# Kernel optimization log

Hardware: AMD Instinct MI355X
Metric: run time of the kernel (lower is better)

Reference implementation:

```python
import jax, jax.numpy as jnp
import numpy as np

N = 100000      # num nodes
E = 1600000     # num edges
IN, H, OUT = 128, 64, 64
EPS = 1e-5      # BatchNorm eps


def setup_inputs() -> dict:
    key = jax.random.key(0)
    ks = jax.random.split(key, 12)
    x = jax.random.normal(ks[0], (N, IN), dtype=jnp.float32)
    edge_index = jax.random.randint(ks[1], (2, E), 0, N, dtype=jnp.int64)
    def lin(k, fan_in, fan_out):
        s = 1.0 / np.sqrt(fan_in)
        kw, kb = jax.random.split(k)
        W = jax.random.uniform(kw, (fan_in, fan_out), jnp.float32, -s, s)
        b = jax.random.uniform(kb, (fan_out,), jnp.float32, -s, s)
        return W, b
    W1, b1 = lin(ks[2], IN, H)
    W2, b2 = lin(ks[3], H, H)
    W3, b3 = lin(ks[4], H, OUT)
    g1 = jnp.ones((H,), jnp.float32); beta1 = jnp.zeros((H,), jnp.float32)
    g2 = jnp.ones((H,), jnp.float32); beta2 = jnp.zeros((H,), jnp.float32)
    rm1 = 0.1 * jax.random.normal(ks[5], (H,), jnp.float32)
    rv1 = 1.0 + 0.1 * jax.random.uniform(ks[6], (H,), jnp.float32)
    rm2 = 0.1 * jax.random.normal(ks[7], (H,), jnp.float32)
    rv2 = 1.0 + 0.1 * jax.random.uniform(ks[8], (H,), jnp.float32)
    return dict(x=x, edge_index=edge_index, W1=W1, b1=b1, W2=W2, b2=b2,
                W3=W3, b3=b3, g1=g1, beta1=beta1, rm1=rm1, rv1=rv1,
                g2=g2, beta2=beta2, rm2=rm2, rv2=rv2)


def _gcn_conv(x, W, b, src, dst, edge_coef, self_coef):
    # x' = D^{-1/2}(A+I)D^{-1/2} (x W) + b   (GCNConv with self-loops)
    h = x @ W                                           # [N, F_out]
    msgs = h[src] * edge_coef[:, None]                  # gather + scale [E, F_out]
    agg = jax.ops.segment_sum(msgs, dst, num_segments=N)  # scatter-add
    return agg + h * self_coef[:, None] + b


def _bn_eval(x, g, beta, rm, rv):
    return (x - rm) * jax.lax.rsqrt(rv + EPS) * g + beta


def reference(x, edge_index, W1, b1, W2, b2, W3, b3,
              g1, beta1, rm1, rv1, g2, beta2, rm2, rv2):
    src, dst = edge_index[0], edge_index[1]
    # symmetric normalization coefficients (deg includes self-loop)
    deg = jax.ops.segment_sum(jnp.ones((E,), x.dtype), dst, num_segments=N) + 1.0
    dinv = jax.lax.rsqrt(deg)
    edge_coef = dinv[src] * dinv[dst]   # [E]
    self_coef = dinv * dinv             # [N]

    h = _gcn_conv(x, W1, b1, src, dst, edge_coef, self_coef)
    h = jax.nn.relu(_bn_eval(h, g1, beta1, rm1, rv1))   # dropout = identity (eval)
    h = _gcn_conv(h, W2, b2, src, dst, edge_coef, self_coef)
    h = jax.nn.relu(_bn_eval(h, g2, beta2, rm2, rv2))
    return _gcn_conv(h, W3, b3, src, dst, edge_coef, self_coef)
```

## Files before the change

### kernel.cpp

```cpp
#include <hip/hip_runtime.h>
#include <hip/hip_fp16.h>

#define NN 100000
#define EE 1600000
#define K1 128
#define HH 64

#define NB 196
#define BW 512
#define CAP 12288
#define CHUNK 4096


__global__ void k_zeroB(int* __restrict__ bcursor) {
    bcursor[threadIdx.x] = 0;
}

__global__ __launch_bounds__(256) void k_binA(const int* __restrict__ ei,
                                              int* __restrict__ bcursor,
                                              uint2* __restrict__ binned) {
    __shared__ int lh[256], lbase[256], lcur[256];
    int t = threadIdx.x;
    int e0 = blockIdx.x * CHUNK;
    int e1 = min(e0 + CHUNK, EE);
    lh[t] = 0;
    __syncthreads();
    for (int e = e0 + t; e < e1; e += 256) {
        int d = ei[EE + e];
        atomicAdd(&lh[d >> 9], 1);
    }
    __syncthreads();
    lbase[t] = (lh[t] > 0) ? atomicAdd(&bcursor[t], lh[t]) : 0;
    lcur[t] = 0;
    __syncthreads();
    for (int e = e0 + t; e < e1; e += 256) {
        int s = ei[e];
        int d = ei[EE + e];
        int b = d >> 9;
        int pos = lbase[b] + atomicAdd(&lcur[b], 1);
        binned[(size_t)b * CAP + pos] = make_uint2((unsigned)s, (unsigned)d);
    }
}

__global__ __launch_bounds__(256) void k_sortB(const uint2* __restrict__ binned,
                                               const int* __restrict__ bcursor,
                                               int* __restrict__ offsets,
                                               float* __restrict__ dinv,
                                               int* __restrict__ csr_src) {
    __shared__ int lhist[BW], excl[BW], lcur[BW];
    __shared__ int sbase_sm;
    int t = threadIdx.x;
    int b = blockIdx.x;
    int lo = b << 9;
    int cnt = bcursor[b];

    lcur[t] = (t < b) ? bcursor[t] : 0;
    __syncthreads();
    for (int off = 128; off > 0; off >>= 1) {
        if (t < off) lcur[t] += lcur[t + off];
        __syncthreads();
    }
    if (t == 0) sbase_sm = lcur[0];
    for (int j = t; j < BW; j += 256) lhist[j] = 0;
    __syncthreads();
    int sbase = sbase_sm;
    const uint2* bp = binned + (size_t)b * CAP;
    for (int i = t; i < cnt; i += 256)
        atomicAdd(&lhist[bp[i].y - lo], 1);
    __syncthreads();
    if (t < 64) {
        int v[8], s = 0;
#pragma unroll
        for (int i = 0; i < 8; i++) { v[i] = lhist[t * 8 + i]; s += v[i]; }
        int run = s;
        for (int off = 1; off < 64; off <<= 1) {
            int u = __shfl_up(run, off);
            if (t >= off) run += u;
        }
        int base = run - s;
#pragma unroll
        for (int i = 0; i < 8; i++) { excl[t * 8 + i] = base; base += v[i]; }
    }
    __syncthreads();
    for (int j = t; j < BW; j += 256) {
        int d = lo + j;
        if (d < NN) {
            offsets[d] = sbase + excl[j];
            dinv[d] = rsqrtf((float)lhist[j] + 1.0f);
        }
    }
    if (b == NB - 1 && t == 0) offsets[NN] = sbase + cnt;
    for (int j = t; j < BW; j += 256) lcur[j] = 0;
    __syncthreads();
    for (int i = t; i < cnt; i += 256) {
        uint2 u = bp[i];
        int d = (int)u.y - lo;
        int slot = excl[d] + atomicAdd(&lcur[d], 1);
        csr_src[sbase + slot] = (int)u.x;
    }
}


template <int K, int TM, bool INH>
__global__ __launch_bounds__(256) void k_gemm(const void* __restrict__ xin,
                                              const float* __restrict__ W,
                                              __half* __restrict__ h) {
    __shared__ float Wl[K * 64];
    __shared__ float xs[TM * K];
    int t = threadIdx.x;
    int base = blockIdx.x * TM;
    for (int i = t; i < K * 16; i += 256)
        reinterpret_cast<float4*>(Wl)[i] = reinterpret_cast<const float4*>(W)[i];
    {
        const int NF4 = TM * K / 4;
        const int RF4 = K / 4;
        for (int i = t; i < NF4; i += 256) {
            int r = i / RF4, c = i - r * RF4;
            int gr = base + r; if (gr >= NN) gr = NN - 1;
            float4 v;
            if (INH) {
                uint2 u = reinterpret_cast<const uint2*>(xin)[(size_t)gr * RF4 + c];
                const __half2* hh = reinterpret_cast<const __half2*>(&u);
                float2 f01 = __half22float2(hh[0]);
                float2 f23 = __half22float2(hh[1]);
                v = make_float4(f01.x, f01.y, f23.x, f23.y);
            } else {
                v = reinterpret_cast<const float4*>(xin)[(size_t)gr * RF4 + c];
            }
            reinterpret_cast<float4*>(xs)[i] = v;
        }
    }
    __syncthreads();

    int lane = t & 63;
    int wid = t >> 6;
    const int RW = TM / 4;
    int r0 = wid * RW;
    float acc[RW];
#pragma unroll
    for (int r = 0; r < RW; r++) acc[r] = 0.f;

    for (int k = 0; k < K; k += 4) {
        float w0 = Wl[(k + 0) * 64 + lane];
        float w1 = Wl[(k + 1) * 64 + lane];
        float w2 = Wl[(k + 2) * 64 + lane];
        float w3 = Wl[(k + 3) * 64 + lane];
#pragma unroll
        for (int r = 0; r < RW; r++) {
            const float4 xv = *reinterpret_cast<const float4*>(&xs[(r0 + r) * K + k]);
            acc[r] = fmaf(xv.x, w0, acc[r]);
            acc[r] = fmaf(xv.y, w1, acc[r]);
            acc[r] = fmaf(xv.z, w2, acc[r]);
            acc[r] = fmaf(xv.w, w3, acc[r]);
        }
    }
    __half* hp = h + ((size_t)base + r0) * 64 + lane;
#pragma unroll
    for (int r = 0; r < RW; r++)
        if (base + r0 + r < NN) hp[r * 64] = __float2half(acc[r]);
}


template <bool BN, bool OUTH>
__global__ __launch_bounds__(256) void k_agg(const __half* __restrict__ h,
                                             const int* __restrict__ csr_src,
                                             const int* __restrict__ offsets,
                                             const float* __restrict__ dinv,
                                             const float* __restrict__ bias,
                                             const float* __restrict__ g,
                                             const float* __restrict__ beta,
                                             const float* __restrict__ rm,
                                             const float* __restrict__ rv,
                                             void* __restrict__ outp) {
    int node = (blockIdx.x * 256 + threadIdx.x) >> 6;
    int lane = threadIdx.x & 63;
    int q = lane >> 4;
    int p = lane & 15;
    int start = offsets[node];
    int len = offsets[node + 1] - start;
    const int* ep = csr_src + start;
    const uint2* hp = reinterpret_cast<const uint2*>(h);

    float a0 = 0.f, a1 = 0.f, a2 = 0.f, a3 = 0.f;
    int i = 0;
    for (; i + 16 <= len; i += 16) {
        uint2 dv[4]; float cf[4];
#pragma unroll
        for (int s = 0; s < 4; s++) {
            int srcn = __builtin_nontemporal_load(ep + i + 4 * q + s);
            cf[s] = dinv[srcn];
            dv[s] = hp[(size_t)srcn * 16 + p];
        }
#pragma unroll
        for (int s = 0; s < 4; s++) {
            const __half2* hh = reinterpret_cast<const __half2*>(&dv[s]);
            float2 f01 = __half22float2(hh[0]);
            float2 f23 = __half22float2(hh[1]);
            a0 = fmaf(f01.x, cf[s], a0);
            a1 = fmaf(f01.y, cf[s], a1);
            a2 = fmaf(f23.x, cf[s], a2);
            a3 = fmaf(f23.y, cf[s], a3);
        }
    }
    if (i < len) {
        uint2 dv[4]; float cf[4];
#pragma unroll
        for (int s = 0; s < 4; s++) {
            int slot = i + 4 * q + s;
            int cl = slot < len ? slot : len - 1;
            int srcn = __builtin_nontemporal_load(ep + cl);
            cf[s] = (slot < len) ? dinv[srcn] : 0.f;
            dv[s] = hp[(size_t)srcn * 16 + p];
        }
#pragma unroll
        for (int s = 0; s < 4; s++) {
            const __half2* hh = reinterpret_cast<const __half2*>(&dv[s]);
            float2 f01 = __half22float2(hh[0]);
            float2 f23 = __half22float2(hh[1]);
            a0 = fmaf(f01.x, cf[s], a0);
            a1 = fmaf(f01.y, cf[s], a1);
            a2 = fmaf(f23.x, cf[s], a2);
            a3 = fmaf(f23.y, cf[s], a3);
        }
    }
    a0 += __shfl_xor(a0, 16); a0 += __shfl_xor(a0, 32);
    a1 += __shfl_xor(a1, 16); a1 += __shfl_xor(a1, 32);
    a2 += __shfl_xor(a2, 16); a2 += __shfl_xor(a2, 32);
    a3 += __shfl_xor(a3, 16); a3 += __shfl_xor(a3, 32);

    if (q == 0) {
        uint2 sv = hp[(size_t)node * 16 + p];
        const __half2* sh = reinterpret_cast<const __half2*>(&sv);
        float2 s01 = __half22float2(sh[0]);
        float2 s23 = __half22float2(sh[1]);
        float di = dinv[node];
        float d2 = di * di;
        float4 bi = reinterpret_cast<const float4*>(bias)[p];
        float r0 = fmaf(s01.x, d2, a0 * di) + bi.x;
        float r1 = fmaf(s01.y, d2, a1 * di) + bi.y;
        float r2 = fmaf(s23.x, d2, a2 * di) + bi.z;
        float r3 = fmaf(s23.y, d2, a3 * di) + bi.w;
        if (BN) {
            float4 gv = reinterpret_cast<const float4*>(g)[p];
            float4 bv = reinterpret_cast<const float4*>(beta)[p];
            float4 mv = reinterpret_cast<const float4*>(rm)[p];
            float4 vv = reinterpret_cast<const float4*>(rv)[p];
            r0 = fmaxf(fmaf(r0 - mv.x, gv.x * rsqrtf(vv.x + 1e-5f), bv.x), 0.f);
            r1 = fmaxf(fmaf(r1 - mv.y, gv.y * rsqrtf(vv.y + 1e-5f), bv.y), 0.f);
            r2 = fmaxf(fmaf(r2 - mv.z, gv.z * rsqrtf(vv.z + 1e-5f), bv.z), 0.f);
            r3 = fmaxf(fmaf(r3 - mv.w, gv.w * rsqrtf(vv.w + 1e-5f), bv.w), 0.f);
        }
        if (OUTH) {
            __half2 o01, o23;
            o01.x = __float2half_rn(r0); o01.y = __float2half_rn(r1);
            o23.x = __float2half_rn(r2); o23.y = __float2half_rn(r3);
            uint2 o;
            o.x = *reinterpret_cast<unsigned*>(&o01);
            o.y = *reinterpret_cast<unsigned*>(&o23);
            reinterpret_cast<uint2*>(outp)[(size_t)node * 16 + p] = o;
        } else {
            float4 o = make_float4(r0, r1, r2, r3);
            reinterpret_cast<float4*>(outp)[(size_t)node * 16 + p] = o;
        }
    }
}


extern "C" void kernel_launch(void* const* d_in, const int* in_sizes, int n_in,
                              void* d_out, int out_size, void* d_ws, size_t ws_size,
                              hipStream_t stream) {
    const float* x = (const float*)d_in[0];
    const int* ei = (const int*)d_in[1];
    const float* W1 = (const float*)d_in[2];
    const float* b1 = (const float*)d_in[3];
    const float* W2 = (const float*)d_in[4];
    const float* b2 = (const float*)d_in[5];
    const float* W3 = (const float*)d_in[6];
    const float* b3 = (const float*)d_in[7];
    const float* g1 = (const float*)d_in[8];
    const float* be1 = (const float*)d_in[9];
    const float* rm1 = (const float*)d_in[10];
    const float* rv1 = (const float*)d_in[11];
    const float* g2 = (const float*)d_in[12];
    const float* be2 = (const float*)d_in[13];
    const float* rm2 = (const float*)d_in[14];
    const float* rv2 = (const float*)d_in[15];
    float* out = (float*)d_out;

    char* ws = (char*)d_ws;
    size_t off = 0;
    auto alloc = [&](size_t bytes) -> void* {
        void* p = ws + off;
        off = (off + bytes + 255) & ~(size_t)255;
        return p;
    };
    int* bcursor = (int*)alloc(256 * 4);
    int* offsets = (int*)alloc((size_t)(NN + 1) * 4);
    float* dinv = (float*)alloc((size_t)NN * 4);
    uint2* binned = (uint2*)alloc((size_t)NB * CAP * 8);
    int* csr_src = (int*)alloc((size_t)EE * 4);
    __half* h16 = (__half*)alloc((size_t)NN * 64 * 2);
    __half* y16 = (__half*)alloc((size_t)NN * 64 * 2);

    k_zeroB<<<1, 256, 0, stream>>>(bcursor);
    k_binA<<<(EE + CHUNK - 1) / CHUNK, 256, 0, stream>>>(ei, bcursor, binned);
    k_sortB<<<NB, 256, 0, stream>>>(binned, bcursor, offsets, dinv, csr_src);

    k_gemm<K1, 32, false><<<NN / 32, 256, 0, stream>>>(x, W1, h16);
    k_agg<true, true><<<NN * 64 / 256, 256, 0, stream>>>(h16, csr_src, offsets, dinv,
                                                         b1, g1, be1, rm1, rv1, y16);
    k_gemm<HH, 64, true><<<(NN + 63) / 64, 256, 0, stream>>>(y16, W2, h16);
    k_agg<true, true><<<NN * 64 / 256, 256, 0, stream>>>(h16, csr_src, offsets, dinv,
                                                         b2, g2, be2, rm2, rv2, y16);
    k_gemm<HH, 64, true><<<(NN + 63) / 64, 256, 0, stream>>>(y16, W3, h16);
    k_agg<false, false><<<NN * 64 / 256, 256, 0, stream>>>(h16, csr_src, offsets, dinv,
                                                           b3, b3, b3, b3, b3, out);
}
```

Before: 340.3 us.

## Fold dinv into GEMM output, widen gather loads, pack binned edges

```diff
diff --git a/kernel.cpp b/kernel.cpp
--- a/kernel.cpp
+++ b/kernel.cpp
@@ -18,31 +18,34 @@
 
 __global__ __launch_bounds__(256) void k_binA(const int* __restrict__ ei,
                                               int* __restrict__ bcursor,
-                                              uint2* __restrict__ binned) {
+                                              unsigned* __restrict__ binned) {
+    __shared__ int ls[CHUNK];
+    __shared__ int ld[CHUNK];
     __shared__ int lh[256], lbase[256], lcur[256];
     int t = threadIdx.x;
     int e0 = blockIdx.x * CHUNK;
-    int e1 = min(e0 + CHUNK, EE);
+    int n = min(CHUNK, EE - e0);
     lh[t] = 0;
     __syncthreads();
-    for (int e = e0 + t; e < e1; e += 256) {
-        int d = ei[EE + e];
+    for (int j = t; j < n; j += 256) {
+        int s = ei[e0 + j];
+        int d = ei[EE + e0 + j];
+        ls[j] = s; ld[j] = d;
         atomicAdd(&lh[d >> 9], 1);
     }
     __syncthreads();
     lbase[t] = (lh[t] > 0) ? atomicAdd(&bcursor[t], lh[t]) : 0;
     lcur[t] = 0;
     __syncthreads();
-    for (int e = e0 + t; e < e1; e += 256) {
-        int s = ei[e];
-        int d = ei[EE + e];
+    for (int j = t; j < n; j += 256) {
+        int d = ld[j];
         int b = d >> 9;
         int pos = lbase[b] + atomicAdd(&lcur[b], 1);
-        binned[(size_t)b * CAP + pos] = make_uint2((unsigned)s, (unsigned)d);
-    }
-}
-
-__global__ __launch_bounds__(256) void k_sortB(const uint2* __restrict__ binned,
+        binned[(size_t)b * CAP + pos] = ((unsigned)(d & 511) << 17) | (unsigned)ls[j];
+    }
+}
+
+__global__ __launch_bounds__(256) void k_sortB(const unsigned* __restrict__ binned,
                                                const int* __restrict__ bcursor,
                                                int* __restrict__ offsets,
                                                float* __restrict__ dinv,
@@ -64,9 +67,9 @@
     for (int j = t; j < BW; j += 256) lhist[j] = 0;
     __syncthreads();
     int sbase = sbase_sm;
-    const uint2* bp = binned + (size_t)b * CAP;
+    const unsigned* bp = binned + (size_t)b * CAP;
     for (int i = t; i < cnt; i += 256)
-        atomicAdd(&lhist[bp[i].y - lo], 1);
+        atomicAdd(&lhist[bp[i] >> 17], 1);
     __syncthreads();
     if (t < 64) {
         int v[8], s = 0;
@@ -93,10 +96,10 @@
     for (int j = t; j < BW; j += 256) lcur[j] = 0;
     __syncthreads();
     for (int i = t; i < cnt; i += 256) {
-        uint2 u = bp[i];
-        int d = (int)u.y - lo;
+        unsigned u = bp[i];
+        int d = (int)(u >> 17);
         int slot = excl[d] + atomicAdd(&lcur[d], 1);
-        csr_src[sbase + slot] = (int)u.x;
+        csr_src[sbase + slot] = (int)(u & 0x1FFFF);
     }
 }
 
@@ -104,6 +107,7 @@
 template <int K, int TM, bool INH>
 __global__ __launch_bounds__(256) void k_gemm(const void* __restrict__ xin,
                                               const float* __restrict__ W,
+                                              const float* __restrict__ dinv,
                                               __half* __restrict__ h) {
     __shared__ float Wl[K * 64];
     __shared__ float xs[TM * K];
@@ -156,8 +160,10 @@
     }
     __half* hp = h + ((size_t)base + r0) * 64 + lane;
 #pragma unroll
-    for (int r = 0; r < RW; r++)
-        if (base + r0 + r < NN) hp[r * 64] = __float2half(acc[r]);
+    for (int r = 0; r < RW; r++) {
+        int row = base + r0 + r;
+        if (row < NN) hp[r * 64] = __float2half(acc[r] * dinv[row]);
+    }
 }
 
 
@@ -174,93 +180,112 @@
                                              void* __restrict__ outp) {
     int node = (blockIdx.x * 256 + threadIdx.x) >> 6;
     int lane = threadIdx.x & 63;
-    int q = lane >> 4;
-    int p = lane & 15;
+    int grp = lane >> 3;
+    int p = lane & 7;
     int start = offsets[node];
     int len = offsets[node + 1] - start;
     const int* ep = csr_src + start;
-    const uint2* hp = reinterpret_cast<const uint2*>(h);
+    const uint4* hp4 = reinterpret_cast<const uint4*>(h);
 
     float a0 = 0.f, a1 = 0.f, a2 = 0.f, a3 = 0.f;
+    float a4 = 0.f, a5 = 0.f, a6 = 0.f, a7 = 0.f;
     int i = 0;
     for (; i + 16 <= len; i += 16) {
-        uint2 dv[4]; float cf[4];
-#pragma unroll
-        for (int s = 0; s < 4; s++) {
-            int srcn = __builtin_nontemporal_load(ep + i + 4 * q + s);
-            cf[s] = dinv[srcn];
-            dv[s] = hp[(size_t)srcn * 16 + p];
-        }
-#pragma unroll
-        for (int s = 0; s < 4; s++) {
-            const __half2* hh = reinterpret_cast<const __half2*>(&dv[s]);
-            float2 f01 = __half22float2(hh[0]);
-            float2 f23 = __half22float2(hh[1]);
-            a0 = fmaf(f01.x, cf[s], a0);
-            a1 = fmaf(f01.y, cf[s], a1);
-            a2 = fmaf(f23.x, cf[s], a2);
-            a3 = fmaf(f23.y, cf[s], a3);
-        }
+        int s0 = __builtin_nontemporal_load(ep + i + 2 * grp);
+        int s1 = __builtin_nontemporal_load(ep + i + 2 * grp + 1);
+        uint4 d0 = hp4[(size_t)s0 * 8 + p];
+        uint4 d1 = hp4[(size_t)s1 * 8 + p];
+        const __half2* h0 = reinterpret_cast<const __half2*>(&d0);
+        const __half2* h1 = reinterpret_cast<const __half2*>(&d1);
+        __half2 q0 = __hadd2(h0[0], h1[0]);
+        __half2 q1 = __hadd2(h0[1], h1[1]);
+        __half2 q2 = __hadd2(h0[2], h1[2]);
+        __half2 q3 = __hadd2(h0[3], h1[3]);
+        float2 f;
+        f = __half22float2(q0); a0 += f.x; a1 += f.y;
+        f = __half22float2(q1); a2 += f.x; a3 += f.y;
+        f = __half22float2(q2); a4 += f.x; a5 += f.y;
+        f = __half22float2(q3); a6 += f.x; a7 += f.y;
     }
     if (i < len) {
-        uint2 dv[4]; float cf[4];
-#pragma unroll
-        for (int s = 0; s < 4; s++) {
-            int slot = i + 4 * q + s;
-            int cl = slot < len ? slot : len - 1;
-            int srcn = __builtin_nontemporal_load(ep + cl);
-            cf[s] = (slot < len) ? dinv[srcn] : 0.f;
-            dv[s] = hp[(size_t)srcn * 16 + p];
-        }
-#pragma unroll
-        for (int s = 0; s < 4; s++) {
-            const __half2* hh = reinterpret_cast<const __half2*>(&dv[s]);
-            float2 f01 = __half22float2(hh[0]);
-            float2 f23 = __half22float2(hh[1]);
-            a0 = fmaf(f01.x, cf[s], a0);
-            a1 = fmaf(f01.y, cf[s], a1);
-            a2 = fmaf(f23.x, cf[s], a2);
-            a3 = fmaf(f23.y, cf[s], a3);
-        }
-    }
-    a0 += __shfl_xor(a0, 16); a0 += __shfl_xor(a0, 32);
-    a1 += __shfl_xor(a1, 16); a1 += __shfl_xor(a1, 32);
-    a2 += __shfl_xor(a2, 16); a2 += __shfl_xor(a2, 32);
-    a3 += __shfl_xor(a3, 16); a3 += __shfl_xor(a3, 32);
-
-    if (q == 0) {
-        uint2 sv = hp[(size_t)node * 16 + p];
-        const __half2* sh = reinterpret_cast<const __half2*>(&sv);
-        float2 s01 = __half22float2(sh[0]);
-        float2 s23 = __half22float2(sh[1]);
+        int e0 = i + 2 * grp, e1 = e0 + 1;
+        int c0 = e0 < len ? e0 : len - 1;
+        int c1 = e1 < len ? e1 : len - 1;
+        int s0 = __builtin_nontemporal_load(ep + c0);
+        int s1 = __builtin_nontemporal_load(ep + c1);
+        uint4 d0 = hp4[(size_t)s0 * 8 + p];
+        uint4 d1 = hp4[(size_t)s1 * 8 + p];
+        if (e0 >= len) d0 = make_uint4(0u, 0u, 0u, 0u);
+        if (e1 >= len) d1 = make_uint4(0u, 0u, 0u, 0u);
+        const __half2* h0 = reinterpret_cast<const __half2*>(&d0);
+        const __half2* h1 = reinterpret_cast<const __half2*>(&d1);
+        __half2 q0 = __hadd2(h0[0], h1[0]);
+        __half2 q1 = __hadd2(h0[1], h1[1]);
+        __half2 q2 = __hadd2(h0[2], h1[2]);
+        __half2 q3 = __hadd2(h0[3], h1[3]);
+        float2 f;
+        f = __half22float2(q0); a0 += f.x; a1 += f.y;
+        f = __half22float2(q1); a2 += f.x; a3 += f.y;
+        f = __half22float2(q2); a4 += f.x; a5 += f.y;
+        f = __half22float2(q3); a6 += f.x; a7 += f.y;
+    }
+#pragma unroll
+    for (int d = 8; d <= 32; d <<= 1) {
+        a0 += __shfl_xor(a0, d); a1 += __shfl_xor(a1, d);
+        a2 += __shfl_xor(a2, d); a3 += __shfl_xor(a3, d);
+        a4 += __shfl_xor(a4, d); a5 += __shfl_xor(a5, d);
+        a6 += __shfl_xor(a6, d); a7 += __shfl_xor(a7, d);
+    }
+
+    if (grp == 0) {
+        uint4 sd = hp4[(size_t)node * 8 + p];
+        const __half2* sh = reinterpret_cast<const __half2*>(&sd);
+        float2 f;
+        f = __half22float2(sh[0]); a0 += f.x; a1 += f.y;
+        f = __half22float2(sh[1]); a2 += f.x; a3 += f.y;
+        f = __half22float2(sh[2]); a4 += f.x; a5 += f.y;
+        f = __half22float2(sh[3]); a6 += f.x; a7 += f.y;
         float di = dinv[node];
-        float d2 = di * di;
-        float4 bi = reinterpret_cast<const float4*>(bias)[p];
-        float r0 = fmaf(s01.x, d2, a0 * di) + bi.x;
-        float r1 = fmaf(s01.y, d2, a1 * di) + bi.y;
-        float r2 = fmaf(s23.x, d2, a2 * di) + bi.z;
-        float r3 = fmaf(s23.y, d2, a3 * di) + bi.w;
+        float4 b0 = reinterpret_cast<const float4*>(bias)[2 * p];
+        float4 b1 = reinterpret_cast<const float4*>(bias)[2 * p + 1];
+        float r0 = fmaf(a0, di, b0.x), r1 = fmaf(a1, di, b0.y);
+        float r2 = fmaf(a2, di, b0.z), r3 = fmaf(a3, di, b0.w);
+        float r4 = fmaf(a4, di, b1.x), r5 = fmaf(a5, di, b1.y);
+        float r6 = fmaf(a6, di, b1.z), r7 = fmaf(a7, di, b1.w);
         if (BN) {
-            float4 gv = reinterpret_cast<const float4*>(g)[p];
-            float4 bv = reinterpret_cast<const float4*>(beta)[p];
-            float4 mv = reinterpret_cast<const float4*>(rm)[p];
-            float4 vv = reinterpret_cast<const float4*>(rv)[p];
-            r0 = fmaxf(fmaf(r0 - mv.x, gv.x * rsqrtf(vv.x + 1e-5f), bv.x), 0.f);
-            r1 = fmaxf(fmaf(r1 - mv.y, gv.y * rsqrtf(vv.y + 1e-5f), bv.y), 0.f);
-            r2 = fmaxf(fmaf(r2 - mv.z, gv.z * rsqrtf(vv.z + 1e-5f), bv.z), 0.f);
-            r3 = fmaxf(fmaf(r3 - mv.w, gv.w * rsqrtf(vv.w + 1e-5f), bv.w), 0.f);
+            float4 g0 = reinterpret_cast<const float4*>(g)[2 * p];
+            float4 g1 = reinterpret_cast<const float4*>(g)[2 * p + 1];
+            float4 t0 = reinterpret_cast<const float4*>(beta)[2 * p];
+            float4 t1 = reinterpret_cast<const float4*>(beta)[2 * p + 1];
+            float4 m0 = reinterpret_cast<const float4*>(rm)[2 * p];
+            float4 m1 = reinterpret_cast<const float4*>(rm)[2 * p + 1];
+            float4 v0 = reinterpret_cast<const float4*>(rv)[2 * p];
+            float4 v1 = reinterpret_cast<const float4*>(rv)[2 * p + 1];
+            r0 = fmaxf(fmaf(r0 - m0.x, g0.x * rsqrtf(v0.x + 1e-5f), t0.x), 0.f);
+            r1 = fmaxf(fmaf(r1 - m0.y, g0.y * rsqrtf(v0.y + 1e-5f), t0.y), 0.f);
+            r2 = fmaxf(fmaf(r2 - m0.z, g0.z * rsqrtf(v0.z + 1e-5f), t0.z), 0.f);
+            r3 = fmaxf(fmaf(r3 - m0.w, g0.w * rsqrtf(v0.w + 1e-5f), t0.w), 0.f);
+            r4 = fmaxf(fmaf(r4 - m1.x, g1.x * rsqrtf(v1.x + 1e-5f), t1.x), 0.f);
+            r5 = fmaxf(fmaf(r5 - m1.y, g1.y * rsqrtf(v1.y + 1e-5f), t1.y), 0.f);
+            r6 = fmaxf(fmaf(r6 - m1.z, g1.z * rsqrtf(v1.z + 1e-5f), t1.z), 0.f);
+            r7 = fmaxf(fmaf(r7 - m1.w, g1.w * rsqrtf(v1.w + 1e-5f), t1.w), 0.f);
         }
         if (OUTH) {
-            __half2 o01, o23;
-            o01.x = __float2half_rn(r0); o01.y = __float2half_rn(r1);
-            o23.x = __float2half_rn(r2); o23.y = __float2half_rn(r3);
-            uint2 o;
-            o.x = *reinterpret_cast<unsigned*>(&o01);
-            o.y = *reinterpret_cast<unsigned*>(&o23);
-            reinterpret_cast<uint2*>(outp)[(size_t)node * 16 + p] = o;
+            __half2 o0; o0.x = __float2half_rn(r0); o0.y = __float2half_rn(r1);
+            __half2 o1; o1.x = __float2half_rn(r2); o1.y = __float2half_rn(r3);
+            __half2 o2; o2.x = __float2half_rn(r4); o2.y = __float2half_rn(r5);
+            __half2 o3; o3.x = __float2half_rn(r6); o3.y = __float2half_rn(r7);
+            uint4 o;
+            o.x = *reinterpret_cast<unsigned*>(&o0);
+            o.y = *reinterpret_cast<unsigned*>(&o1);
+            o.z = *reinterpret_cast<unsigned*>(&o2);
+            o.w = *reinterpret_cast<unsigned*>(&o3);
+            reinterpret_cast<uint4*>(outp)[(size_t)node * 8 + p] = o;
         } else {
-            float4 o = make_float4(r0, r1, r2, r3);
-            reinterpret_cast<float4*>(outp)[(size_t)node * 16 + p] = o;
+            reinterpret_cast<float4*>(outp)[(size_t)node * 16 + 2 * p] =
+                make_float4(r0, r1, r2, r3);
+            reinterpret_cast<float4*>(outp)[(size_t)node * 16 + 2 * p + 1] =
+                make_float4(r4, r5, r6, r7);
         }
     }
 }
@@ -297,7 +322,7 @@
     int* bcursor = (int*)alloc(256 * 4);
     int* offsets = (int*)alloc((size_t)(NN + 1) * 4);
     float* dinv = (float*)alloc((size_t)NN * 4);
-    uint2* binned = (uint2*)alloc((size_t)NB * CAP * 8);
+    unsigned* binned = (unsigned*)alloc((size_t)NB * CAP * 4);
     int* csr_src = (int*)alloc((size_t)EE * 4);
     __half* h16 = (__half*)alloc((size_t)NN * 64 * 2);
     __half* y16 = (__half*)alloc((size_t)NN * 64 * 2);
@@ -306,13 +331,13 @@
     k_binA<<<(EE + CHUNK - 1) / CHUNK, 256, 0, stream>>>(ei, bcursor, binned);
     k_sortB<<<NB, 256, 0, stream>>>(binned, bcursor, offsets, dinv, csr_src);
 
-    k_gemm<K1, 32, false><<<NN / 32, 256, 0, stream>>>(x, W1, h16);
+    k_gemm<K1, 32, false><<<NN / 32, 256, 0, stream>>>(x, W1, dinv, h16);
     k_agg<true, true><<<NN * 64 / 256, 256, 0, stream>>>(h16, csr_src, offsets, dinv,
                                                          b1, g1, be1, rm1, rv1, y16);
-    k_gemm<HH, 64, true><<<(NN + 63) / 64, 256, 0, stream>>>(y16, W2, h16);
+    k_gemm<HH, 64, true><<<(NN + 63) / 64, 256, 0, stream>>>(y16, W2, dinv, h16);
     k_agg<true, true><<<NN * 64 / 256, 256, 0, stream>>>(h16, csr_src, offsets, dinv,
                                                          b2, g2, be2, rm2, rv2, y16);
-    k_gemm<HH, 64, true><<<(NN + 63) / 64, 256, 0, stream>>>(y16, W3, h16);
+    k_gemm<HH, 64, true><<<(NN + 63) / 64, 256, 0, stream>>>(y16, W3, dinv, h16);
     k_agg<false, false><<<NN * 64 / 256, 256, 0, stream>>>(h16, csr_src, offsets, dinv,
                                                            b3, b3, b3, b3, b3, out);
 }
```

Result: faster. 325.8 us (-4.3%).
